# Kernel optimization log

Measured on AMD Instinct MI355X. Metric: run time of the kernel, lower is better.

The kernel has to match this reference:

```python
import jax, jax.numpy as jnp
import numpy as np

B, S, F_IN, E = 8, 1024, 256, 512
INNER = 2 * E            # mLSTM proj_factor = 2.0
NH = 4                   # mLSTM num_heads
DH = INNER // NH
KS = 4                   # causal conv1d kernel size
QKV_BS = 4               # qkv_proj_blocksize
NB = INNER // QKV_BS     # number of block-diagonal qkv blocks


def setup_inputs() -> dict:
    key = jax.random.key(0)
    ks = jax.random.split(key, 16)
    g = lambda k, shape, scale: jax.random.normal(k, shape, jnp.float32) * scale
    return {
        "x": g(ks[0], (B, S, F_IN), 1.0),
        "W_in": g(ks[1], (E, F_IN), F_IN ** -0.5),
        "b_in": jnp.zeros((E,), jnp.float32),
        "ln1_w": jnp.ones((E,), jnp.float32),
        "W_up": g(ks[2], (2 * INNER, E), E ** -0.5),
        "conv_w": g(ks[3], (INNER, 1, KS), KS ** -0.5),
        "conv_b": jnp.zeros((INNER,), jnp.float32),
        "Wq": g(ks[4], (NB, QKV_BS, QKV_BS), QKV_BS ** -0.5),
        "Wk": g(ks[5], (NB, QKV_BS, QKV_BS), QKV_BS ** -0.5),
        "Wv": g(ks[6], (NB, QKV_BS, QKV_BS), QKV_BS ** -0.5),
        "W_ig": g(ks[7], (NH, 3 * INNER), (3 * INNER) ** -0.5),
        "b_ig": jnp.zeros((NH,), jnp.float32),
        "W_fg": g(ks[8], (NH, 3 * INNER), (3 * INNER) ** -0.5),
        "b_fg": jnp.linspace(3.0, 6.0, NH, dtype=jnp.float32),  # xlstm fgate bias init
        "mhln_w": jnp.ones((INNER,), jnp.float32),
        "skip": jnp.ones((INNER,), jnp.float32),
        "W_down": g(ks[9], (E, INNER), INNER ** -0.5),
        "ln_post_w": jnp.ones((E,), jnp.float32),
    }


def _ln(h, w, eps=1e-5):
    m = h.mean(-1, keepdims=True)
    v = jnp.mean((h - m) ** 2, axis=-1, keepdims=True)
    return (h - m) * jax.lax.rsqrt(v + eps) * w


def _causal_conv(x, w, b):
    # x: (B,S,C) -> depthwise causal conv, kernel KS, left-pad KS-1
    y = jax.lax.conv_general_dilated(
        x.transpose(0, 2, 1), w, (1,), [(KS - 1, 0)],
        dimension_numbers=("NCH", "OIH", "NCH"), feature_group_count=INNER)
    return y.transpose(0, 2, 1) + b


def _headwise(x, W):
    # block-diagonal linear (LinearHeadwiseExpand, bias=False)
    b, s, _ = x.shape
    xh = x.reshape(b, s, NB, QKV_BS)
    return jnp.einsum("bsni,noi->bsno", xh, W).reshape(b, s, -1)


def reference(x, W_in, b_in, ln1_w, W_up, conv_w, conv_b, Wq, Wk, Wv,
              W_ig, b_ig, W_fg, b_fg, mhln_w, skip, W_down, ln_post_w):
    # input proj (+ dropout = identity in eval)
    xp = x @ W_in.T + b_in                                  # (B,S,E)
    res = xp
    h = _ln(xp, ln1_w)                                      # pre-LN of mLSTM block
    up = h @ W_up.T                                         # (B,S,2*INNER)
    x_m, z = up[..., :INNER], up[..., INNER:]
    xc = jax.nn.silu(_causal_conv(x_m, conv_w, conv_b))     # (B,S,INNER)
    q = _headwise(xc, Wq)
    k = _headwise(xc, Wk)
    v = _headwise(x_m, Wv)
    gate_in = jnp.concatenate([q, k, v], axis=-1)           # (B,S,3*INNER)
    ig = (gate_in @ W_ig.T + b_ig).transpose(0, 2, 1)       # (B,NH,S)
    fg = (gate_in @ W_fg.T + b_fg).transpose(0, 2, 1)       # (B,NH,S)
    to_h = lambda t: t.reshape(B, S, NH, DH).transpose(0, 2, 1, 3)
    qh, kh, vh = to_h(q), to_h(k), to_h(v)                  # (B,NH,S,DH)
    # --- parallel_stabilized_simple mLSTM backend ---
    logf = jax.nn.log_sigmoid(fg)                           # (B,NH,S)
    a = jnp.concatenate([jnp.zeros_like(logf[..., :1]), jnp.cumsum(logf, -1)], -1)
    M = a[..., :, None] - a[..., None, :]                   # (B,NH,S+1,S+1)
    mask = jnp.tril(jnp.ones((S + 1, S + 1), bool))
    logD = jnp.where(mask, M, -jnp.inf)[..., 1:, 1:] + ig[..., None, :]
    maxD = logD.max(-1, keepdims=True)                      # (B,NH,S,1)
    D = jnp.exp(logD - maxD)
    C = jnp.einsum("bnsd,bntd->bnst", qh, kh * (DH ** -0.5)) * D
    n = jnp.maximum(jnp.abs(C.sum(-1, keepdims=True)), jnp.exp(-maxD))
    hh = jnp.einsum("bnst,bntd->bnsd", C / (n + 1e-6), vh)  # (B,NH,S,DH)
    # multi-head layernorm (GroupNorm per head, weight only, bias-free)
    hn = hh.transpose(0, 2, 1, 3)                           # (B,S,NH,DH)
    mu = hn.mean(-1, keepdims=True)
    var = jnp.mean((hn - mu) ** 2, axis=-1, keepdims=True)
    hn = (hn - mu) * jax.lax.rsqrt(var + 1e-5) * mhln_w.reshape(NH, DH)
    hn = hn.reshape(B, S, INNER)
    h_state = (hn + skip * xc) * jax.nn.silu(z)             # learnable skip + output gate
    y = h_state @ W_down.T                                  # (B,S,E)
    out = res + y                                           # residual
    return _ln(out, ln_post_w)                              # post_blocks_norm
```

## Files before the change

### kernel.cpp

```cpp
#include <hip/hip_runtime.h>

#define S_LEN 1024
#define B_SZ 8
#define F_IN_D 256
#define E_DIM 512
#define INNER_D 1024
#define NH_D 4
#define DH_D 256
#define NROW (B_SZ * S_LEN)

typedef _Float16 half8 __attribute__((ext_vector_type(8)));
typedef _Float16 half4_t __attribute__((ext_vector_type(4)));
typedef float v4f __attribute__((ext_vector_type(4)));

__global__ __launch_bounds__(256) void cast4_kernel(
    const float* __restrict__ s0, const float* __restrict__ s1,
    const float* __restrict__ s2, const float* __restrict__ s3,
    _Float16* __restrict__ d0, _Float16* __restrict__ d1,
    _Float16* __restrict__ d2, _Float16* __restrict__ d3,
    int n0, int n1, int n2, int n3)
{
  int i = (blockIdx.x * 256 + threadIdx.x) * 4;
  const float* s; _Float16* d; int off;
  if (i < n0)                { s = s0; d = d0; off = i; }
  else if (i < n0 + n1)      { s = s1; d = d1; off = i - n0; }
  else if (i < n0 + n1 + n2) { s = s2; d = d2; off = i - n0 - n1; }
  else if (i < n0 + n1 + n2 + n3) { s = s3; d = d3; off = i - n0 - n1 - n2; }
  else return;
  float4 v = *(const float4*)(s + off);
  half4_t o = {(_Float16)v.x, (_Float16)v.y, (_Float16)v.z, (_Float16)v.w};
  *(half4_t*)(d + off) = o;
}

#define GBM 128
#define GBN 128
#define GBK 32
#define LDKG (GBK + 8)

__global__ __launch_bounds__(256) void gemm_h16(
    const _Float16* __restrict__ A, const _Float16* __restrict__ B,
    const float* __restrict__ bias, float* __restrict__ C,
    int M, int N, int K)
{
  __shared__ __align__(16) _Float16 As[GBM][LDKG];
  __shared__ __align__(16) _Float16 Bs[GBN][LDKG];
  const int tid = threadIdx.x;
  const int lane = tid & 63, w = tid >> 6;
  const int wr = w >> 1, wc = w & 1;
  const int quad = lane >> 4, l16 = lane & 15;
  const int bm = blockIdx.y * GBM, bn = blockIdx.x * GBN;
  const int srow = tid >> 1;
  const int scol = (tid & 1) * 16;

  v4f acc[4][4];
#pragma unroll
  for (int i = 0; i < 4; ++i)
#pragma unroll
    for (int j = 0; j < 4; ++j) acc[i][j] = (v4f){0.f, 0.f, 0.f, 0.f};

  const _Float16* Ap = A + (size_t)(bm + srow) * K + scol;
  const _Float16* Bp = B + (size_t)(bn + srow) * K + scol;
  half8 a0 = *(const half8*)(Ap);
  half8 a1 = *(const half8*)(Ap + 8);
  half8 b0 = *(const half8*)(Bp);
  half8 b1 = *(const half8*)(Bp + 8);

  for (int k0 = 0; k0 < K; k0 += GBK) {
    __syncthreads();
    *(half8*)(&As[srow][scol]) = a0;
    *(half8*)(&As[srow][scol + 8]) = a1;
    *(half8*)(&Bs[srow][scol]) = b0;
    *(half8*)(&Bs[srow][scol + 8]) = b1;
    __syncthreads();
    if (k0 + GBK < K) {
      const int kn = k0 + GBK;
      a0 = *(const half8*)(Ap + kn);
      a1 = *(const half8*)(Ap + kn + 8);
      b0 = *(const half8*)(Bp + kn);
      b1 = *(const half8*)(Bp + kn + 8);
    }
    half8 af[4], bf[4];
#pragma unroll
    for (int i = 0; i < 4; ++i)
      af[i] = *(const half8*)(&As[wr * 64 + i * 16 + l16][quad * 8]);
#pragma unroll
    for (int j = 0; j < 4; ++j)
      bf[j] = *(const half8*)(&Bs[wc * 64 + j * 16 + l16][quad * 8]);
#pragma unroll
    for (int i = 0; i < 4; ++i)
#pragma unroll
      for (int j = 0; j < 4; ++j)
        acc[i][j] = __builtin_amdgcn_mfma_f32_16x16x32_f16(af[i], bf[j], acc[i][j], 0, 0, 0);
  }

#pragma unroll
  for (int j = 0; j < 4; ++j) {
    const int col = bn + wc * 64 + j * 16 + l16;
    const float bv = bias ? bias[col] : 0.f;
#pragma unroll
    for (int i = 0; i < 4; ++i) {
      const int row0 = bm + wr * 64 + i * 16 + quad * 4;
#pragma unroll
      for (int r = 0; r < 4; ++r)
        C[(size_t)(row0 + r) * N + col] = acc[i][j][r] + bv;
    }
  }
}

__global__ __launch_bounds__(256) void gemm_h16_up(
    const _Float16* __restrict__ A, const _Float16* __restrict__ B,
    _Float16* __restrict__ xmh, _Float16* __restrict__ szb,
    int M, int N, int K)
{
  __shared__ __align__(16) _Float16 As[GBM][LDKG];
  __shared__ __align__(16) _Float16 Bs[GBN][LDKG];
  const int tid = threadIdx.x;
  const int lane = tid & 63, w = tid >> 6;
  const int wr = w >> 1, wc = w & 1;
  const int quad = lane >> 4, l16 = lane & 15;
  const int bm = blockIdx.y * GBM, bn = blockIdx.x * GBN;
  const int srow = tid >> 1;
  const int scol = (tid & 1) * 16;

  v4f acc[4][4];
#pragma unroll
  for (int i = 0; i < 4; ++i)
#pragma unroll
    for (int j = 0; j < 4; ++j) acc[i][j] = (v4f){0.f, 0.f, 0.f, 0.f};

  const _Float16* Ap = A + (size_t)(bm + srow) * K + scol;
  const _Float16* Bp = B + (size_t)(bn + srow) * K + scol;
  half8 a0 = *(const half8*)(Ap);
  half8 a1 = *(const half8*)(Ap + 8);
  half8 b0 = *(const half8*)(Bp);
  half8 b1 = *(const half8*)(Bp + 8);

  for (int k0 = 0; k0 < K; k0 += GBK) {
    __syncthreads();
    *(half8*)(&As[srow][scol]) = a0;
    *(half8*)(&As[srow][scol + 8]) = a1;
    *(half8*)(&Bs[srow][scol]) = b0;
    *(half8*)(&Bs[srow][scol + 8]) = b1;
    __syncthreads();
    if (k0 + GBK < K) {
      const int kn = k0 + GBK;
      a0 = *(const half8*)(Ap + kn);
      a1 = *(const half8*)(Ap + kn + 8);
      b0 = *(const half8*)(Bp + kn);
      b1 = *(const half8*)(Bp + kn + 8);
    }
    half8 af[4], bf[4];
#pragma unroll
    for (int i = 0; i < 4; ++i)
      af[i] = *(const half8*)(&As[wr * 64 + i * 16 + l16][quad * 8]);
#pragma unroll
    for (int j = 0; j < 4; ++j)
      bf[j] = *(const half8*)(&Bs[wc * 64 + j * 16 + l16][quad * 8]);
#pragma unroll
    for (int i = 0; i < 4; ++i)
#pragma unroll
      for (int j = 0; j < 4; ++j)
        acc[i][j] = __builtin_amdgcn_mfma_f32_16x16x32_f16(af[i], bf[j], acc[i][j], 0, 0, 0);
  }

  const bool zhalf = (bn >= INNER_D);
#pragma unroll
  for (int j = 0; j < 4; ++j) {
    const int col = bn + wc * 64 + j * 16 + l16;
    const int colm = col & (INNER_D - 1);
#pragma unroll
    for (int i = 0; i < 4; ++i) {
      const int row0 = bm + wr * 64 + i * 16 + quad * 4;
#pragma unroll
      for (int r = 0; r < 4; ++r) {
        float a = acc[i][j][r];
        if (zhalf) {
          float s = a / (1.f + __expf(-a));
          szb[(size_t)(row0 + r) * INNER_D + colm] = (_Float16)s;
        } else {
          xmh[(size_t)(row0 + r) * INNER_D + colm] = (_Float16)a;
        }
      }
    }
  }
}

__device__ __forceinline__ float block_sum4(float v, float* red, int tid) {
#pragma unroll
  for (int off = 32; off; off >>= 1) v += __shfl_xor(v, off);
  if ((tid & 63) == 0) red[tid >> 6] = v;
  __syncthreads();
  float t = red[0] + red[1] + red[2] + red[3];
  __syncthreads();
  return t;
}

__global__ __launch_bounds__(256) void ln_mul_kernel(
    const float* __restrict__ in, const float* __restrict__ w,
    _Float16* __restrict__ out)
{
  __shared__ float red[4];
  const int row = blockIdx.x;
  const int tid = threadIdx.x;
  const float* p = in + (size_t)row * E_DIM;
  float v0 = p[tid], v1 = p[tid + 256];
  float mean = block_sum4(v0 + v1, red, tid) * (1.f / E_DIM);
  float d0 = v0 - mean, d1 = v1 - mean;
  float var = block_sum4(d0 * d0 + d1 * d1, red, tid) * (1.f / E_DIM);
  float rstd = rsqrtf(var + 1e-5f);
  out[(size_t)row * E_DIM + tid] = (_Float16)(d0 * rstd * w[tid]);
  out[(size_t)row * E_DIM + tid + 256] = (_Float16)(d1 * rstd * w[tid + 256]);
}

__global__ __launch_bounds__(256) void final_ln_kernel(
    const float* __restrict__ res, const float* __restrict__ y,
    const float* __restrict__ w, float* __restrict__ out)
{
  __shared__ float red[4];
  const int row = blockIdx.x;
  const int tid = threadIdx.x;
  const size_t base = (size_t)row * E_DIM;
  float v0 = res[base + tid] + y[base + tid];
  float v1 = res[base + tid + 256] + y[base + tid + 256];
  float mean = block_sum4(v0 + v1, red, tid) * (1.f / E_DIM);
  float d0 = v0 - mean, d1 = v1 - mean;
  float var = block_sum4(d0 * d0 + d1 * d1, red, tid) * (1.f / E_DIM);
  float rstd = rsqrtf(var + 1e-5f);
  out[base + tid] = d0 * rstd * w[tid];
  out[base + tid + 256] = d1 * rstd * w[tid + 256];
}

__global__ __launch_bounds__(256) void chg_kernel(
    const _Float16* __restrict__ xm, const float* __restrict__ cw,
    const float* __restrict__ cb,
    const float* __restrict__ Wq, const float* __restrict__ Wk,
    const float* __restrict__ Wv,
    const float* __restrict__ Wig, const float* __restrict__ big,
    const float* __restrict__ Wfg, const float* __restrict__ bfg,
    _Float16* __restrict__ xch, _Float16* __restrict__ qh,
    _Float16* __restrict__ khb, _Float16* __restrict__ vhb,
    float* __restrict__ ig, float* __restrict__ fg)
{
  __shared__ float red[4][32];
  const int tid = threadIdx.x;
  const int lane = tid & 63, wid = tid >> 6;
  const int row0 = blockIdx.x * 4;
  const int sl0 = row0 & (S_LEN - 1);
  const int c = tid * 4;

  float t[7][4];
#pragma unroll
  for (int j = 0; j < 7; ++j) {
    const int off = j - 3;
    if (sl0 + off < 0) {
      t[j][0] = t[j][1] = t[j][2] = t[j][3] = 0.f;
    } else {
      half4_t hv = *(const half4_t*)(xm + (size_t)(row0 + off) * INNER_D + c);
      t[j][0] = (float)hv.x; t[j][1] = (float)hv.y;
      t[j][2] = (float)hv.z; t[j][3] = (float)hv.w;
    }
  }
  float wct[4][4];
#pragma unroll
  for (int j = 0; j < 4; ++j) {
    float4 wc4 = *(const float4*)(cw + (c + j) * 4);
    wct[j][0] = wc4.x; wct[j][1] = wc4.y; wct[j][2] = wc4.z; wct[j][3] = wc4.w;
  }
  float4 cb4 = *(const float4*)(cb + c);
  const float cbs[4] = {cb4.x, cb4.y, cb4.z, cb4.w};
  float wqm[16], wkm[16], wvm[16];
#pragma unroll
  for (int i = 0; i < 4; ++i) {
    float4 a = *(const float4*)(Wq + tid * 16 + i * 4);
    float4 bq = *(const float4*)(Wk + tid * 16 + i * 4);
    float4 cq = *(const float4*)(Wv + tid * 16 + i * 4);
    wqm[i * 4] = a.x; wqm[i * 4 + 1] = a.y; wqm[i * 4 + 2] = a.z; wqm[i * 4 + 3] = a.w;
    wkm[i * 4] = bq.x; wkm[i * 4 + 1] = bq.y; wkm[i * 4 + 2] = bq.z; wkm[i * 4 + 3] = bq.w;
    wvm[i * 4] = cq.x; wvm[i * 4 + 1] = cq.y; wvm[i * 4 + 2] = cq.z; wvm[i * 4 + 3] = cq.w;
  }

  float q4[4][4], k4[4][4], v4m[4][4];
#pragma unroll
  for (int r = 0; r < 4; ++r) {
    float xc4[4];
#pragma unroll
    for (int j = 0; j < 4; ++j) {
      float a = cbs[j] + wct[j][0] * t[r][j] + wct[j][1] * t[r + 1][j]
                       + wct[j][2] * t[r + 2][j] + wct[j][3] * t[r + 3][j];
      xc4[j] = a / (1.f + __expf(-a));
    }
#pragma unroll
    for (int i = 0; i < 4; ++i) {
      q4[r][i] = wqm[i * 4] * xc4[0] + wqm[i * 4 + 1] * xc4[1]
               + wqm[i * 4 + 2] * xc4[2] + wqm[i * 4 + 3] * xc4[3];
      k4[r][i] = wkm[i * 4] * xc4[0] + wkm[i * 4 + 1] * xc4[1]
               + wkm[i * 4 + 2] * xc4[2] + wkm[i * 4 + 3] * xc4[3];
      v4m[r][i] = wvm[i * 4] * t[r + 3][0] + wvm[i * 4 + 1] * t[r + 3][1]
                + wvm[i * 4 + 2] * t[r + 3][2] + wvm[i * 4 + 3] * t[r + 3][3];
    }
    const size_t base = (size_t)(row0 + r) * INNER_D + c;
    half4_t xo = {(_Float16)xc4[0], (_Float16)xc4[1], (_Float16)xc4[2], (_Float16)xc4[3]};
    half4_t qo = {(_Float16)q4[r][0], (_Float16)q4[r][1], (_Float16)q4[r][2], (_Float16)q4[r][3]};
    half4_t ko = {(_Float16)k4[r][0], (_Float16)k4[r][1], (_Float16)k4[r][2], (_Float16)k4[r][3]};
    half4_t vo = {(_Float16)v4m[r][0], (_Float16)v4m[r][1], (_Float16)v4m[r][2], (_Float16)v4m[r][3]};
    *(half4_t*)(xch + base) = xo;
    *(half4_t*)(qh + base) = qo;
    *(half4_t*)(khb + base) = ko;
    *(half4_t*)(vhb + base) = vo;
  }

  float vals[32];
#pragma unroll
  for (int g = 0; g < 8; ++g) {
    const float* wb = (g < 4 ? Wig : Wfg) + (g & 3) * 3072 + c;
    float4 w1 = *(const float4*)(wb);
    float4 w2 = *(const float4*)(wb + 1024);
    float4 w3 = *(const float4*)(wb + 2048);
#pragma unroll
    for (int r = 0; r < 4; ++r) {
      vals[g * 4 + r] =
          q4[r][0] * w1.x + q4[r][1] * w1.y + q4[r][2] * w1.z + q4[r][3] * w1.w
        + k4[r][0] * w2.x + k4[r][1] * w2.y + k4[r][2] * w2.z + k4[r][3] * w2.w
        + v4m[r][0] * w3.x + v4m[r][1] * w3.y + v4m[r][2] * w3.z + v4m[r][3] * w3.w;
    }
  }
#pragma unroll
  for (int i = 0; i < 32; ++i) {
    float x = vals[i];
#pragma unroll
    for (int off = 32; off; off >>= 1) x += __shfl_xor(x, off);
    vals[i] = x;
  }
  if (lane == 0) {
#pragma unroll
    for (int i = 0; i < 32; ++i) red[wid][i] = vals[i];
  }
  __syncthreads();
  if (tid < 32) {
    float sm = red[0][tid] + red[1][tid] + red[2][tid] + red[3][tid];
    const int g = tid >> 2, r = tid & 3;
    const int h = g & 3;
    const int b = row0 >> 10;
    const size_t oidx = (size_t)(b * NH_D + h) * S_LEN + sl0 + r;
    if (g < 4) ig[oidx] = sm + big[h];
    else       fg[oidx] = sm + bfg[h];
  }
}

__device__ __forceinline__ float logsigf(float x) {
  return fminf(x, 0.f) - log1pf(__expf(-fabsf(x)));
}

__global__ __launch_bounds__(256) void scan_kernel(
    const float* __restrict__ ig, const float* __restrict__ fg,
    float* __restrict__ m_, float* __restrict__ rmax_, float* __restrict__ maxd_,
    float* __restrict__ em_)
{
  __shared__ float sc[256];
  const int bh = blockIdx.x;
  const int tid = threadIdx.x;
  const size_t base = (size_t)bh * S_LEN + tid * 4;
  float4 f4 = *(const float4*)(fg + base);
  float4 i4 = *(const float4*)(ig + base);
  float l0 = logsigf(f4.x), l1 = logsigf(f4.y), l2 = logsigf(f4.z), l3 = logsigf(f4.w);
  float p0 = l0, p1 = p0 + l1, p2 = p1 + l2, p3 = p2 + l3;
  sc[tid] = p3;
  __syncthreads();
  for (int off = 1; off < 256; off <<= 1) {
    float o = (tid >= off) ? sc[tid - off] : 0.f;
    __syncthreads();
    sc[tid] += o;
    __syncthreads();
  }
  float aoff = (tid == 0) ? 0.f : sc[tid - 1];
  __syncthreads();
  float a0 = aoff + p0, a1 = aoff + p1, a2 = aoff + p2, a3 = aoff + p3;
  float m0 = i4.x - a0, m1 = i4.y - a1, m2 = i4.z - a2, m3 = i4.w - a3;
  float x0 = m0, x1 = fmaxf(x0, m1), x2 = fmaxf(x1, m2), x3 = fmaxf(x2, m3);
  sc[tid] = x3;
  __syncthreads();
  for (int off = 1; off < 256; off <<= 1) {
    float o = (tid >= off) ? sc[tid - off] : -1e30f;
    __syncthreads();
    sc[tid] = fmaxf(sc[tid], o);
    __syncthreads();
  }
  float moff = (tid == 0) ? -1e30f : sc[tid - 1];
  float tmax = sc[tid | 15];
  float r0 = fmaxf(moff, x0), r1 = fmaxf(moff, x1), r2 = fmaxf(moff, x2), r3 = fmaxf(moff, x3);
  const float scale = 0.0625f;
  float4 mo = {m0, m1, m2, m3};
  float4 ro = {r0, r1, r2, r3};
  float4 dd = {a0 + r0, a1 + r1, a2 + r2, a3 + r3};
  float4 eo = {scale * __expf(m0 - tmax), scale * __expf(m1 - tmax),
               scale * __expf(m2 - tmax), scale * __expf(m3 - tmax)};
  *(float4*)(m_ + base) = mo;
  *(float4*)(rmax_ + base) = ro;
  *(float4*)(maxd_ + base) = dd;
  *(float4*)(em_ + base) = eo;
}

__global__ __launch_bounds__(256) void vtrans_kernel(
    const _Float16* __restrict__ vb, _Float16* __restrict__ vt)
{
  __shared__ _Float16 tile[64][68];
  const int b = blockIdx.z, dt = blockIdx.x, st = blockIdx.y;
  const int c4 = (threadIdx.x & 15) * 4, rr = threadIdx.x >> 4;
  const int s0 = st * 64, d0 = dt * 64;
#pragma unroll
  for (int i = 0; i < 4; ++i) {
    int r = rr + i * 16;
    half4_t v = *(const half4_t*)(vb + ((size_t)(b * S_LEN + s0 + r)) * INNER_D + d0 + c4);
    tile[r][c4 + 0] = v.x; tile[r][c4 + 1] = v.y;
    tile[r][c4 + 2] = v.z; tile[r][c4 + 3] = v.w;
  }
  __syncthreads();
#pragma unroll
  for (int i = 0; i < 4; ++i) {
    int dd = rr + i * 16;
    half4_t o = {tile[c4 + 0][dd], tile[c4 + 1][dd], tile[c4 + 2][dd], tile[c4 + 3][dd]};
    *(half4_t*)(vt + ((size_t)(b * INNER_D + d0 + dd)) * S_LEN + s0 + c4) = o;
  }
}

#define KP 264
#define VP 72

__global__ __launch_bounds__(256, 2) void attn_blk_kernel(
    const _Float16* __restrict__ qh, const _Float16* __restrict__ khb,
    const _Float16* __restrict__ vt,
    const float* __restrict__ m_, const float* __restrict__ em,
    const float* __restrict__ rmax_, const float* __restrict__ maxd_,
    const float* __restrict__ mhln_w, const float* __restrict__ skip,
    const _Float16* __restrict__ xch, const _Float16* __restrict__ szb,
    _Float16* __restrict__ hstate)
{
  __shared__ __align__(16) _Float16 Ks[64][KP];
  __shared__ __align__(16) _Float16 Vs[256][VP];
  __shared__ _Float16 plds[4][16][72];
  const int tid = threadIdx.x;
  const int lane = tid & 63, wid = tid >> 6;
  const int quad = lane >> 4, l16 = lane & 15;
  const int bh = blockIdx.x & 31;
  const int pp = blockIdx.x >> 5;
  const int sblk = 15 - pp;
  const int h = bh & 3, b = bh >> 2;
  _Float16 (*P)[72] = plds[wid];
  const float* rmaxp = rmax_ + (size_t)bh * S_LEN;
  const float* emp = em + (size_t)bh * S_LEN;
  const float* mp = m_ + (size_t)bh * S_LEN;
  const float* maxdp = maxd_ + (size_t)bh * S_LEN;
  const float scale = 0.0625f;

  const _Float16* kg = khb + ((size_t)(b * S_LEN)) * INNER_D + h * DH_D;
  const _Float16* vg = vt + ((size_t)(b * INNER_D + h * DH_D)) * S_LEN;
  const int krow_s = tid >> 5;
  const int kcol_s = (tid & 31) * 8;
  const int vrow_s = tid >> 3;
  const int vcol_s = (tid & 7) * 8;

  const int ntile = sblk + 1;
  const int s0 = sblk * 64 + wid * 16;

  half8 kpre[8], vpre[8];
#pragma unroll
  for (int i = 0; i < 8; ++i) {
    kpre[i] = *(const half8*)(kg + (size_t)(i * 8 + krow_s) * INNER_D + kcol_s);
    vpre[i] = *(const half8*)(vg + (size_t)(i * 32 + vrow_s) * S_LEN + vcol_s);
  }

  half8 qf[8];
  const _Float16* qrow = qh + ((size_t)(b * S_LEN + s0 + l16)) * INNER_D + h * DH_D + quad * 8;
#pragma unroll
  for (int c = 0; c < 8; ++c) qf[c] = *(const half8*)(qrow + c * 32);

  v4f acc[16];
#pragma unroll
  for (int nc = 0; nc < 16; ++nc) acc[nc] = (v4f){0.f, 0.f, 0.f, 0.f};
  float rsum[4] = {0.f, 0.f, 0.f, 0.f};
  float rmax_row[4];
#pragma unroll
  for (int r = 0; r < 4; ++r) rmax_row[r] = rmaxp[s0 + quad * 4 + r];

  for (int tt = 0; tt < ntile; ++tt) {
    const int t0 = tt * 64;
    const bool last = (tt + 1 == ntile);
    __syncthreads();
#pragma unroll
    for (int i = 0; i < 8; ++i) {
      *(half8*)(&Ks[i * 8 + krow_s][kcol_s]) = kpre[i];
      *(half8*)(&Vs[i * 32 + vrow_s][vcol_s]) = vpre[i];
    }
    __syncthreads();
    if (!last) {
      const int tn = t0 + 64;
#pragma unroll
      for (int i = 0; i < 8; ++i) {
        kpre[i] = *(const half8*)(kg + (size_t)(tn + i * 8 + krow_s) * INNER_D + kcol_s);
        vpre[i] = *(const half8*)(vg + (size_t)(i * 32 + vrow_s) * S_LEN + tn + vcol_s);
      }
    }
    const bool diag = last;
    float rowfac[4];
    if (!diag) {
      const float rtile = rmaxp[t0 + 63];
#pragma unroll
      for (int r = 0; r < 4; ++r) rowfac[r] = __expf(rtile - rmax_row[r]);
    }
#pragma unroll
    for (int sub = 0; sub < 4; ++sub) {
      v4f sacc0 = (v4f){0.f, 0.f, 0.f, 0.f};
      v4f sacc1 = (v4f){0.f, 0.f, 0.f, 0.f};
#pragma unroll
      for (int c = 0; c < 4; ++c) {
        half8 kf0 = *(const half8*)(&Ks[sub * 16 + l16][c * 32 + quad * 8]);
        half8 kf1 = *(const half8*)(&Ks[sub * 16 + l16][(c + 4) * 32 + quad * 8]);
        sacc0 = __builtin_amdgcn_mfma_f32_16x16x32_f16(qf[c], kf0, sacc0, 0, 0, 0);
        sacc1 = __builtin_amdgcn_mfma_f32_16x16x32_f16(qf[c + 4], kf1, sacc1, 0, 0, 0);
      }
      v4f sacc = sacc0 + sacc1;
      const int t = t0 + sub * 16 + l16;
      if (diag) {
        const float mt = mp[t];
#pragma unroll
        for (int r = 0; r < 4; ++r) {
          const int srow = s0 + quad * 4 + r;
          float cc = (t <= srow) ? sacc[r] * scale * __expf(mt - rmax_row[r]) : 0.f;
          rsum[r] += cc;
          P[quad * 4 + r][sub * 16 + l16] = (_Float16)cc;
        }
      } else {
        const float emv = emp[t];
#pragma unroll
        for (int r = 0; r < 4; ++r) {
          float cc = sacc[r] * emv * rowfac[r];
          rsum[r] += cc;
          P[quad * 4 + r][sub * 16 + l16] = (_Float16)cc;
        }
      }
    }
    asm volatile("s_waitcnt lgkmcnt(0)" ::: "memory");
    half8 pf0 = *(const half8*)(&P[l16][quad * 8]);
    half8 pf1 = *(const half8*)(&P[l16][32 + quad * 8]);
#pragma unroll
    for (int nc = 0; nc < 16; ++nc) {
      half8 vf0 = *(const half8*)(&Vs[nc * 16 + l16][quad * 8]);
      half8 vf1 = *(const half8*)(&Vs[nc * 16 + l16][32 + quad * 8]);
      acc[nc] = __builtin_amdgcn_mfma_f32_16x16x32_f16(pf0, vf0, acc[nc], 0, 0, 0);
      acc[nc] = __builtin_amdgcn_mfma_f32_16x16x32_f16(pf1, vf1, acc[nc], 0, 0, 0);
    }
  }

  float inv[4];
#pragma unroll
  for (int r = 0; r < 4; ++r) {
    float rs = rsum[r];
    rs += __shfl_xor(rs, 1); rs += __shfl_xor(rs, 2);
    rs += __shfl_xor(rs, 4); rs += __shfl_xor(rs, 8);
    float md = maxdp[s0 + quad * 4 + r];
    float n = fmaxf(fabsf(rs), __expf(-md));
    inv[r] = 1.f / (n + 1e-6f);
  }
#pragma unroll
  for (int nc = 0; nc < 16; ++nc) {
#pragma unroll
    for (int r = 0; r < 4; ++r) acc[nc][r] *= inv[r];
  }
  float mean[4], rstd[4];
#pragma unroll
  for (int r = 0; r < 4; ++r) {
    float sm = 0.f;
#pragma unroll
    for (int nc = 0; nc < 16; ++nc) sm += acc[nc][r];
    sm += __shfl_xor(sm, 1); sm += __shfl_xor(sm, 2);
    sm += __shfl_xor(sm, 4); sm += __shfl_xor(sm, 8);
    mean[r] = sm * (1.f / DH_D);
  }
#pragma unroll
  for (int r = 0; r < 4; ++r) {
    float sq = 0.f;
#pragma unroll
    for (int nc = 0; nc < 16; ++nc) { float d = acc[nc][r] - mean[r]; sq += d * d; }
    sq += __shfl_xor(sq, 1); sq += __shfl_xor(sq, 2);
    sq += __shfl_xor(sq, 4); sq += __shfl_xor(sq, 8);
    rstd[r] = rsqrtf(sq * (1.f / DH_D) + 1e-5f);
  }
#pragma unroll
  for (int nc = 0; nc < 16; ++nc) {
    const int d = h * DH_D + nc * 16 + l16;
    const float w = mhln_w[d];
    const float sk = skip[d];
#pragma unroll
    for (int r = 0; r < 4; ++r) {
      const size_t row = (size_t)(b * S_LEN + s0 + quad * 4 + r);
      float xcv = (float)xch[row * INNER_D + d];
      float sz = (float)szb[row * INNER_D + d];
      float o = ((acc[nc][r] - mean[r]) * rstd[r] * w + sk * xcv) * sz;
      hstate[row * INNER_D + d] = (_Float16)o;
    }
  }
}

extern "C" void kernel_launch(void* const* d_in, const int* in_sizes, int n_in,
                              void* d_out, int out_size, void* d_ws, size_t ws_size,
                              hipStream_t stream)
{
  const float* x      = (const float*)d_in[0];
  const float* W_in   = (const float*)d_in[1];
  const float* b_in   = (const float*)d_in[2];
  const float* ln1_w  = (const float*)d_in[3];
  const float* W_up   = (const float*)d_in[4];
  const float* conv_w = (const float*)d_in[5];
  const float* conv_b = (const float*)d_in[6];
  const float* Wq     = (const float*)d_in[7];
  const float* Wk     = (const float*)d_in[8];
  const float* Wv     = (const float*)d_in[9];
  const float* W_ig   = (const float*)d_in[10];
  const float* b_ig   = (const float*)d_in[11];
  const float* W_fg   = (const float*)d_in[12];
  const float* b_fg   = (const float*)d_in[13];
  const float* mhln_w = (const float*)d_in[14];
  const float* skip   = (const float*)d_in[15];
  const float* W_down = (const float*)d_in[16];
  const float* ln_post_w = (const float*)d_in[17];
  float* out = (float*)d_out;

  float* ws = (float*)d_ws;
  size_t o = 0;
  float* xp     = ws + o; o += (size_t)NROW * E_DIM;
  float* hbuf   = ws + o; o += (size_t)NROW * E_DIM;
  _Float16* h16 = (_Float16*)(ws + o);
  size_t ho = 0;
  _Float16* xh      = h16 + ho; ho += (size_t)NROW * F_IN_D;
  _Float16* WinH    = h16 + ho; ho += (size_t)E_DIM * F_IN_D;
  _Float16* WupH    = h16 + ho; ho += (size_t)2 * INNER_D * E_DIM;
  _Float16* WdownH  = h16 + ho; ho += (size_t)E_DIM * INNER_D;
  _Float16* hh      = h16 + ho; ho += (size_t)NROW * E_DIM;
  _Float16* xmh     = h16 + ho; ho += (size_t)NROW * INNER_D;
  _Float16* szb     = h16 + ho; ho += (size_t)NROW * INNER_D;
  _Float16* xch     = h16 + ho; ho += (size_t)NROW * INNER_D;
  _Float16* qh      = h16 + ho; ho += (size_t)NROW * INNER_D;
  _Float16* khb     = h16 + ho; ho += (size_t)NROW * INNER_D;
  _Float16* vhb     = h16 + ho; ho += (size_t)NROW * INNER_D;
  _Float16* vtb     = h16 + ho; ho += (size_t)NROW * INNER_D;
  _Float16* hstateH = h16 + ho; ho += (size_t)NROW * INNER_D;

  const int GSZ = B_SZ * NH_D * S_LEN;
  float* igb   = hbuf;
  float* fgb   = hbuf + GSZ;
  float* mb    = hbuf + 2 * GSZ;
  float* rmaxb = hbuf + 3 * GSZ;
  float* maxdb = hbuf + 4 * GSZ;
  float* emb   = hbuf + 5 * GSZ;
  float* yb    = hbuf;

  dim3 blk(256);
  const int nx = NROW * F_IN_D, nwi = E_DIM * F_IN_D,
            nwu = 2 * INNER_D * E_DIM, nwd = E_DIM * INNER_D;
  const int ntot = nx + nwi + nwu + nwd;
  cast4_kernel<<<(ntot / 4 + 255) / 256, blk, 0, stream>>>(
      x, W_in, W_up, W_down, xh, WinH, WupH, WdownH, nx, nwi, nwu, nwd);
  gemm_h16<<<dim3(E_DIM / GBN, NROW / GBM), blk, 0, stream>>>(
      xh, WinH, b_in, xp, NROW, E_DIM, F_IN_D);
  ln_mul_kernel<<<NROW, blk, 0, stream>>>(xp, ln1_w, hh);
  gemm_h16_up<<<dim3(2 * INNER_D / GBN, NROW / GBM), blk, 0, stream>>>(
      hh, WupH, xmh, szb, NROW, 2 * INNER_D, E_DIM);
  chg_kernel<<<NROW / 4, blk, 0, stream>>>(
      xmh, conv_w, conv_b, Wq, Wk, Wv, W_ig, b_ig, W_fg, b_fg,
      xch, qh, khb, vhb, igb, fgb);
  scan_kernel<<<B_SZ * NH_D, blk, 0, stream>>>(igb, fgb, mb, rmaxb, maxdb, emb);
  vtrans_kernel<<<dim3(16, 16, 8), blk, 0, stream>>>(vhb, vtb);
  attn_blk_kernel<<<512, blk, 0, stream>>>(
      qh, khb, vtb, mb, emb, rmaxb, maxdb, mhln_w, skip, xch, szb, hstateH);
  gemm_h16<<<dim3(E_DIM / GBN, NROW / GBM), blk, 0, stream>>>(
      hstateH, WdownH, nullptr, yb, NROW, E_DIM, INNER_D);
  final_ln_kernel<<<NROW, blk, 0, stream>>>(xp, yb, ln_post_w, out);
}
```

Measured before the change: 286.4 us.

## Switch attention kernel to 32x32x16 MFMA with wave pairs splitting columns

Rewrites the chunked mLSTM attention kernel to use 32x32x16 MFMA tiles instead of 16x16x32. Two waves share each 32-row query block: each computes half of the key columns for S, and half of the head dimension for the PV product. Row sums and the layernorm statistics are combined across the pair through shared memory. The intent is fewer MFMA instructions and fewer LDS fragment loads per FLOP, at the cost of extra block-wide syncs and a cross-wave reduction step in the epilogue.

After: 332.3 us. 1.16x slower.

```diff
diff --git a/kernel.cpp b/kernel.cpp
--- a/kernel.cpp
+++ b/kernel.cpp
@@ -12,6 +12,7 @@
 typedef _Float16 half8 __attribute__((ext_vector_type(8)));
 typedef _Float16 half4_t __attribute__((ext_vector_type(4)));
 typedef float v4f __attribute__((ext_vector_type(4)));
+typedef float v16f __attribute__((ext_vector_type(16)));
 
 __global__ __launch_bounds__(256) void cast4_kernel(
     const float* __restrict__ s0, const float* __restrict__ s1,
@@ -426,7 +427,7 @@
 #define KP 264
 #define VP 72
 
-__global__ __launch_bounds__(256, 2) void attn_blk_kernel(
+__global__ __launch_bounds__(256, 2) void attn32_kernel(
     const _Float16* __restrict__ qh, const _Float16* __restrict__ khb,
     const _Float16* __restrict__ vt,
     const float* __restrict__ m_, const float* __restrict__ em,
@@ -437,15 +438,17 @@
 {
   __shared__ __align__(16) _Float16 Ks[64][KP];
   __shared__ __align__(16) _Float16 Vs[256][VP];
-  __shared__ _Float16 plds[4][16][72];
+  __shared__ __align__(16) _Float16 plds[2][32][72];
+  float* redb = (float*)plds;
+
   const int tid = threadIdx.x;
   const int lane = tid & 63, wid = tid >> 6;
-  const int quad = lane >> 4, l16 = lane & 15;
+  const int pair = wid >> 1, hw = wid & 1;
+  const int l31 = lane & 31, hl = lane >> 5;
   const int bh = blockIdx.x & 31;
   const int pp = blockIdx.x >> 5;
   const int sblk = 15 - pp;
   const int h = bh & 3, b = bh >> 2;
-  _Float16 (*P)[72] = plds[wid];
   const float* rmaxp = rmax_ + (size_t)bh * S_LEN;
   const float* emp = em + (size_t)bh * S_LEN;
   const float* mp = m_ + (size_t)bh * S_LEN;
@@ -460,7 +463,11 @@
   const int vcol_s = (tid & 7) * 8;
 
   const int ntile = sblk + 1;
-  const int s0 = sblk * 64 + wid * 16;
+  const int s0 = sblk * 64 + pair * 32;
+
+  int rowl[16];
+#pragma unroll
+  for (int i = 0; i < 16; ++i) rowl[i] = (i & 3) + 8 * (i >> 2) + 4 * hl;
 
   half8 kpre[8], vpre[8];
 #pragma unroll
@@ -469,18 +476,22 @@
     vpre[i] = *(const half8*)(vg + (size_t)(i * 32 + vrow_s) * S_LEN + vcol_s);
   }
 
-  half8 qf[8];
-  const _Float16* qrow = qh + ((size_t)(b * S_LEN + s0 + l16)) * INNER_D + h * DH_D + quad * 8;
-#pragma unroll
-  for (int c = 0; c < 8; ++c) qf[c] = *(const half8*)(qrow + c * 32);
-
-  v4f acc[16];
-#pragma unroll
-  for (int nc = 0; nc < 16; ++nc) acc[nc] = (v4f){0.f, 0.f, 0.f, 0.f};
-  float rsum[4] = {0.f, 0.f, 0.f, 0.f};
-  float rmax_row[4];
-#pragma unroll
-  for (int r = 0; r < 4; ++r) rmax_row[r] = rmaxp[s0 + quad * 4 + r];
+  half8 qf[16];
+  const _Float16* qrow = qh + ((size_t)(b * S_LEN + s0 + l31)) * INNER_D + h * DH_D + hl * 8;
+#pragma unroll
+  for (int kc = 0; kc < 16; ++kc) qf[kc] = *(const half8*)(qrow + kc * 16);
+
+  v16f acc[4];
+#pragma unroll
+  for (int dt = 0; dt < 4; ++dt) acc[dt] = (v16f)(0.f);
+  float rsum[16];
+#pragma unroll
+  for (int i = 0; i < 16; ++i) rsum[i] = 0.f;
+  float rmax_row[16];
+#pragma unroll
+  for (int i = 0; i < 16; ++i) rmax_row[i] = rmaxp[s0 + rowl[i]];
+
+  const int tloc = hw * 32 + l31;
 
   for (int tt = 0; tt < ntile; ++tt) {
     const int t0 = tt * 64;
@@ -500,102 +511,123 @@
         vpre[i] = *(const half8*)(vg + (size_t)(i * 32 + vrow_s) * S_LEN + tn + vcol_s);
       }
     }
+    v16f sa0 = (v16f)(0.f), sa1 = (v16f)(0.f);
+#pragma unroll
+    for (int kc = 0; kc < 8; ++kc) {
+      half8 kf0 = *(const half8*)(&Ks[hw * 32 + l31][kc * 16 + hl * 8]);
+      half8 kf1 = *(const half8*)(&Ks[hw * 32 + l31][(kc + 8) * 16 + hl * 8]);
+      sa0 = __builtin_amdgcn_mfma_f32_32x32x16_f16(qf[kc], kf0, sa0, 0, 0, 0);
+      sa1 = __builtin_amdgcn_mfma_f32_32x32x16_f16(qf[kc + 8], kf1, sa1, 0, 0, 0);
+    }
+    v16f sacc = sa0 + sa1;
+    const int t = t0 + tloc;
     const bool diag = last;
-    float rowfac[4];
-    if (!diag) {
+    if (diag) {
+      const float mt = mp[t];
+#pragma unroll
+      for (int i = 0; i < 16; ++i) {
+        const int srow = s0 + rowl[i];
+        float cc = (t <= srow) ? sacc[i] * scale * __expf(mt - rmax_row[i]) : 0.f;
+        rsum[i] += cc;
+        plds[pair][rowl[i]][tloc] = (_Float16)cc;
+      }
+    } else {
       const float rtile = rmaxp[t0 + 63];
-#pragma unroll
-      for (int r = 0; r < 4; ++r) rowfac[r] = __expf(rtile - rmax_row[r]);
-    }
-#pragma unroll
-    for (int sub = 0; sub < 4; ++sub) {
-      v4f sacc0 = (v4f){0.f, 0.f, 0.f, 0.f};
-      v4f sacc1 = (v4f){0.f, 0.f, 0.f, 0.f};
-#pragma unroll
-      for (int c = 0; c < 4; ++c) {
-        half8 kf0 = *(const half8*)(&Ks[sub * 16 + l16][c * 32 + quad * 8]);
-        half8 kf1 = *(const half8*)(&Ks[sub * 16 + l16][(c + 4) * 32 + quad * 8]);
-        sacc0 = __builtin_amdgcn_mfma_f32_16x16x32_f16(qf[c], kf0, sacc0, 0, 0, 0);
-        sacc1 = __builtin_amdgcn_mfma_f32_16x16x32_f16(qf[c + 4], kf1, sacc1, 0, 0, 0);
+      const float emv = emp[t];
+#pragma unroll
+      for (int i = 0; i < 16; ++i) {
+        float cc = sacc[i] * emv * __expf(rtile - rmax_row[i]);
+        rsum[i] += cc;
+        plds[pair][rowl[i]][tloc] = (_Float16)cc;
       }
-      v4f sacc = sacc0 + sacc1;
-      const int t = t0 + sub * 16 + l16;
-      if (diag) {
-        const float mt = mp[t];
-#pragma unroll
-        for (int r = 0; r < 4; ++r) {
-          const int srow = s0 + quad * 4 + r;
-          float cc = (t <= srow) ? sacc[r] * scale * __expf(mt - rmax_row[r]) : 0.f;
-          rsum[r] += cc;
-          P[quad * 4 + r][sub * 16 + l16] = (_Float16)cc;
-        }
-      } else {
-        const float emv = emp[t];
-#pragma unroll
-        for (int r = 0; r < 4; ++r) {
-          float cc = sacc[r] * emv * rowfac[r];
-          rsum[r] += cc;
-          P[quad * 4 + r][sub * 16 + l16] = (_Float16)cc;
-        }
+    }
+    __syncthreads();
+#pragma unroll
+    for (int kc = 0; kc < 4; ++kc) {
+      half8 pf = *(const half8*)(&plds[pair][l31][kc * 16 + hl * 8]);
+#pragma unroll
+      for (int dt = 0; dt < 4; ++dt) {
+        half8 vf = *(const half8*)(&Vs[hw * 128 + dt * 32 + l31][kc * 16 + hl * 8]);
+        acc[dt] = __builtin_amdgcn_mfma_f32_32x32x16_f16(pf, vf, acc[dt], 0, 0, 0);
       }
     }
-    asm volatile("s_waitcnt lgkmcnt(0)" ::: "memory");
-    half8 pf0 = *(const half8*)(&P[l16][quad * 8]);
-    half8 pf1 = *(const half8*)(&P[l16][32 + quad * 8]);
-#pragma unroll
-    for (int nc = 0; nc < 16; ++nc) {
-      half8 vf0 = *(const half8*)(&Vs[nc * 16 + l16][quad * 8]);
-      half8 vf1 = *(const half8*)(&Vs[nc * 16 + l16][32 + quad * 8]);
-      acc[nc] = __builtin_amdgcn_mfma_f32_16x16x32_f16(pf0, vf0, acc[nc], 0, 0, 0);
-      acc[nc] = __builtin_amdgcn_mfma_f32_16x16x32_f16(pf1, vf1, acc[nc], 0, 0, 0);
-    }
-  }
-
-  float inv[4];
-#pragma unroll
-  for (int r = 0; r < 4; ++r) {
-    float rs = rsum[r];
-    rs += __shfl_xor(rs, 1); rs += __shfl_xor(rs, 2);
-    rs += __shfl_xor(rs, 4); rs += __shfl_xor(rs, 8);
-    float md = maxdp[s0 + quad * 4 + r];
-    float n = fmaxf(fabsf(rs), __expf(-md));
-    inv[r] = 1.f / (n + 1e-6f);
-  }
-#pragma unroll
-  for (int nc = 0; nc < 16; ++nc) {
-#pragma unroll
-    for (int r = 0; r < 4; ++r) acc[nc][r] *= inv[r];
-  }
-  float mean[4], rstd[4];
-#pragma unroll
-  for (int r = 0; r < 4; ++r) {
-    float sm = 0.f;
-#pragma unroll
-    for (int nc = 0; nc < 16; ++nc) sm += acc[nc][r];
-    sm += __shfl_xor(sm, 1); sm += __shfl_xor(sm, 2);
-    sm += __shfl_xor(sm, 4); sm += __shfl_xor(sm, 8);
-    mean[r] = sm * (1.f / DH_D);
-  }
-#pragma unroll
-  for (int r = 0; r < 4; ++r) {
+  }
+
+#pragma unroll
+  for (int i = 0; i < 16; ++i) {
+    float x = rsum[i];
+    x += __shfl_xor(x, 1); x += __shfl_xor(x, 2); x += __shfl_xor(x, 4);
+    x += __shfl_xor(x, 8); x += __shfl_xor(x, 16);
+    rsum[i] = x;
+  }
+  __syncthreads();
+  if (l31 == 0) {
+#pragma unroll
+    for (int i = 0; i < 16; ++i) redb[(pair * 2 + hw) * 32 + rowl[i]] = rsum[i];
+  }
+  __syncthreads();
+  float inv[16];
+#pragma unroll
+  for (int i = 0; i < 16; ++i) {
+    float tot = redb[(pair * 2 + 0) * 32 + rowl[i]] + redb[(pair * 2 + 1) * 32 + rowl[i]];
+    float md = maxdp[s0 + rowl[i]];
+    float n = fmaxf(fabsf(tot), __expf(-md));
+    inv[i] = 1.f / (n + 1e-6f);
+  }
+#pragma unroll
+  for (int dt = 0; dt < 4; ++dt)
+#pragma unroll
+    for (int i = 0; i < 16; ++i) acc[dt][i] *= inv[i];
+  float ps[16];
+#pragma unroll
+  for (int i = 0; i < 16; ++i) {
+    float x = acc[0][i] + acc[1][i] + acc[2][i] + acc[3][i];
+    x += __shfl_xor(x, 1); x += __shfl_xor(x, 2); x += __shfl_xor(x, 4);
+    x += __shfl_xor(x, 8); x += __shfl_xor(x, 16);
+    ps[i] = x;
+  }
+  __syncthreads();
+  if (l31 == 0) {
+#pragma unroll
+    for (int i = 0; i < 16; ++i) redb[(pair * 2 + hw) * 32 + rowl[i]] = ps[i];
+  }
+  __syncthreads();
+  float meanv[16];
+#pragma unroll
+  for (int i = 0; i < 16; ++i)
+    meanv[i] = (redb[(pair * 2) * 32 + rowl[i]] + redb[(pair * 2 + 1) * 32 + rowl[i]]) * (1.f / DH_D);
+  __syncthreads();
+#pragma unroll
+  for (int i = 0; i < 16; ++i) {
     float sq = 0.f;
 #pragma unroll
-    for (int nc = 0; nc < 16; ++nc) { float d = acc[nc][r] - mean[r]; sq += d * d; }
-    sq += __shfl_xor(sq, 1); sq += __shfl_xor(sq, 2);
-    sq += __shfl_xor(sq, 4); sq += __shfl_xor(sq, 8);
-    rstd[r] = rsqrtf(sq * (1.f / DH_D) + 1e-5f);
-  }
-#pragma unroll
-  for (int nc = 0; nc < 16; ++nc) {
-    const int d = h * DH_D + nc * 16 + l16;
+    for (int dt = 0; dt < 4; ++dt) { float d = acc[dt][i] - meanv[i]; sq += d * d; }
+    sq += __shfl_xor(sq, 1); sq += __shfl_xor(sq, 2); sq += __shfl_xor(sq, 4);
+    sq += __shfl_xor(sq, 8); sq += __shfl_xor(sq, 16);
+    ps[i] = sq;
+  }
+  if (l31 == 0) {
+#pragma unroll
+    for (int i = 0; i < 16; ++i) redb[(pair * 2 + hw) * 32 + rowl[i]] = ps[i];
+  }
+  __syncthreads();
+  float rstdv[16];
+#pragma unroll
+  for (int i = 0; i < 16; ++i) {
+    float v = (redb[(pair * 2) * 32 + rowl[i]] + redb[(pair * 2 + 1) * 32 + rowl[i]]) * (1.f / DH_D);
+    rstdv[i] = rsqrtf(v + 1e-5f);
+  }
+#pragma unroll
+  for (int dt = 0; dt < 4; ++dt) {
+    const int d = h * DH_D + hw * 128 + dt * 32 + l31;
     const float w = mhln_w[d];
     const float sk = skip[d];
 #pragma unroll
-    for (int r = 0; r < 4; ++r) {
-      const size_t row = (size_t)(b * S_LEN + s0 + quad * 4 + r);
+    for (int i = 0; i < 16; ++i) {
+      const size_t row = (size_t)(b * S_LEN + s0 + rowl[i]);
       float xcv = (float)xch[row * INNER_D + d];
       float sz = (float)szb[row * INNER_D + d];
-      float o = ((acc[nc][r] - mean[r]) * rstd[r] * w + sk * xcv) * sz;
+      float o = ((acc[dt][i] - meanv[i]) * rstdv[i] * w + sk * xcv) * sz;
       hstate[row * INNER_D + d] = (_Float16)o;
     }
   }
@@ -670,7 +702,7 @@
       xch, qh, khb, vhb, igb, fgb);
   scan_kernel<<<B_SZ * NH_D, blk, 0, stream>>>(igb, fgb, mb, rmaxb, maxdb, emb);
   vtrans_kernel<<<dim3(16, 16, 8), blk, 0, stream>>>(vhb, vtb);
-  attn_blk_kernel<<<512, blk, 0, stream>>>(
+  attn32_kernel<<<512, blk, 0, stream>>>(
       qh, khb, vtb, mb, emb, rmaxb, maxdb, mhln_w, skip, xch, szb, hstateH);
   gemm_h16<<<dim3(E_DIM / GBN, NROW / GBM), blk, 0, stream>>>(
       hstateH, WdownH, nullptr, yb, NROW, E_DIM, INNER_D);
```
